# Performance work log

Hardware: AMD Instinct MI355X
Metric: run time of the kernel (lower is better)

The kernel has to match this reference:

```python
import jax, jax.numpy as jnp
import numpy as np

N = 8192       # number of nodes (dense NxN attention)
F_IN = 256     # input feature dim
F_OUT = 64     # projected feature dim (F_prime)
NEG_SLOPE = 0.01  # nn.LeakyReLU default


def setup_inputs() -> dict:
    key = jax.random.key(0)
    k0, k1, k2, k3 = jax.random.split(key, 4)
    H = jax.random.normal(k0, (N, F_IN), dtype=jnp.float32)
    # dense 0/1 adjacency; force self-loops so every row has a nonzero denominator
    A = jax.random.randint(k1, (N, N), 0, 2, dtype=jnp.int32)
    A = jnp.maximum(A, jnp.eye(N, dtype=jnp.int32))
    # learned params: W : F_IN -> F_OUT (self.W), a : 2*F_OUT -> 1 (self.a)
    W = jax.random.normal(k2, (F_IN, F_OUT), dtype=jnp.float32) / np.sqrt(F_IN)
    bW = jnp.zeros((F_OUT,), dtype=jnp.float32)
    a_w = jax.random.normal(k3, (2 * F_OUT,), dtype=jnp.float32) / np.sqrt(2 * F_OUT)
    a_b = jnp.zeros((), dtype=jnp.float32)
    return {"H": H, "A": A, "W": W, "bW": bW, "a_w": a_w, "a_b": a_b}


def reference(H, A, W, bW, a_w, a_b):
    # Wh[i] = W(H[i])  -> [N, F_OUT]
    Wh = H @ W + bW
    # a([Wh_i ; Wh_j]) = a1.Wh_i + a2.Wh_j + a_b : decompose the concat-linear
    s_src = Wh @ a_w[:F_OUT]           # [N]
    s_tar = Wh @ a_w[F_OUT:]           # [N]
    logits = s_src[:, None] + s_tar[None, :] + a_b   # [N, N]
    # e_ij = exp(leaky_relu(logits))
    e = jnp.exp(jnp.where(logits >= 0, logits, NEG_SLOPE * logits))
    # denominator masks by adjacency (sum_j e_ij * A_ij), as in the original
    denom = jnp.sum(e * A.astype(e.dtype), axis=1, keepdims=True)  # [N, 1]
    alpha = e / denom                   # NOTE: numerator NOT masked (faithful)
    # H'_i = sigmoid(alpha_i @ Wh)
    return jax.nn.sigmoid(alpha @ Wh)   # [N, F_OUT]
```

## Files before the change

### kernel.cpp

```cpp
#include <hip/hip_runtime.h>
#include <hip/hip_bf16.h>

#define NN 8192
#define FIN 256
#define FOUT 64

__global__ __launch_bounds__(256) void k1_proj(
    const float* __restrict__ H, const float* __restrict__ W,
    const float* __restrict__ bW, const float* __restrict__ aw,
    const float* __restrict__ ab,
    float* __restrict__ Wh, float* __restrict__ s_src, float* __restrict__ t_tar,
    float* __restrict__ E1, float* __restrict__ E2, float* __restrict__ PP)
{
    __shared__ float Hs[16 * FIN];
    int tid = threadIdx.x;
    int i0 = blockIdx.x * 16;
    const float4* Hv = (const float4*)(H + (size_t)i0 * FIN);
    float4* Hsv = (float4*)Hs;
    for (int idx = tid; idx < 16 * FIN / 4; idx += 256) Hsv[idx] = Hv[idx];
    __syncthreads();
    int f = tid & 63, sub = tid >> 6;
    float a1f = aw[f], a2f = aw[64 + f];
    float b = bW[f];
    float acc0 = b, acc1 = b, acc2 = b, acc3 = b;
    for (int k = 0; k < FIN; ++k) {
        float w = W[k * FOUT + f];
        acc0 += Hs[(sub     ) * FIN + k] * w;
        acc1 += Hs[(sub +  4) * FIN + k] * w;
        acc2 += Hs[(sub +  8) * FIN + k] * w;
        acc3 += Hs[(sub + 12) * FIN + k] * w;
    }
    float accs[4] = {acc0, acc1, acc2, acc3};
    #pragma unroll
    for (int q = 0; q < 4; ++q) {
        int i = i0 + sub + 4 * q;
        float a = accs[q];
        Wh[(size_t)i * FOUT + f] = a;
        float v1 = a * a1f, v2 = a * a2f;
        #pragma unroll
        for (int o = 32; o > 0; o >>= 1) {
            v1 += __shfl_xor(v1, o);
            v2 += __shfl_xor(v2, o);
        }
        if (f == 0) {
            float s = v1 + ab[0];
            float t = v2;
            s_src[i] = s; t_tar[i] = t;
            E1[i] = __expf(s); E2[i] = __expf(0.01f * s);
            PP[2 * i]     = __expf(t);
            PP[2 * i + 1] = __expf(0.01f * t);
        }
    }
}

__global__ __launch_bounds__(256) void k2_rank(
    const float* __restrict__ t_tar, const float* __restrict__ s_src,
    int* __restrict__ sorted_idx, int* __restrict__ kidx)
{
    __shared__ float Ts[NN];
    int tid = threadIdx.x;
    const float4* tv = (const float4*)t_tar;
    float4* Tsv = (float4*)Ts;
    for (int idx = tid; idx < NN / 4; idx += 256) Tsv[idx] = tv[idx];
    __syncthreads();
    int wv = tid >> 6, lane = tid & 63;
    int g = blockIdx.x * 4 + wv;
    float tj = Ts[g];
    float thr = -s_src[g];
    int rank = 0, kc = 0;
    #pragma unroll 4
    for (int k = lane; k < NN; k += 64) {
        float tk = Ts[k];
        rank += (tk < tj || (tk == tj && k < g)) ? 1 : 0;
        kc   += (tk < thr) ? 1 : 0;
    }
    #pragma unroll
    for (int o = 32; o > 0; o >>= 1) {
        rank += __shfl_xor(rank, o);
        kc   += __shfl_xor(kc, o);
    }
    if (lane == 0) { sorted_idx[rank] = g; kidx[g] = kc; }
}

__global__ __launch_bounds__(64) void k3a_tots(
    const float* __restrict__ Wh, const float* __restrict__ PP,
    const int* __restrict__ sorted_idx,
    float* __restrict__ tots1, float* __restrict__ tots2)
{
    int c = blockIdx.x, f = threadIdx.x;
    float t1 = 0.f, t2 = 0.f;
    int m0 = c * 32;
    #pragma unroll 8
    for (int m = m0; m < m0 + 32; ++m) {
        int sj = sorted_idx[m];
        float wh = Wh[(size_t)sj * 64 + f];
        t1 += PP[2 * sj]     * wh;
        t2 += PP[2 * sj + 1] * wh;
    }
    tots1[c * 64 + f] = t1; tots2[c * 64 + f] = t2;
}

__global__ __launch_bounds__(1024) void k3b_scan(
    const float* __restrict__ tots1, const float* __restrict__ tots2,
    float* __restrict__ off1, float* __restrict__ off2,
    float* __restrict__ pre2, float* __restrict__ suf1)
{
    __shared__ float w1[16 * 64], w2[16 * 64];
    int tid = threadIdx.x, f = tid & 63, wv = tid >> 6;
    int c0 = wv * 16;
    float s1 = 0.f, s2 = 0.f;
    for (int c = c0; c < c0 + 16; ++c) { s1 += tots1[c * 64 + f]; s2 += tots2[c * 64 + f]; }
    w1[wv * 64 + f] = s1; w2[wv * 64 + f] = s2;
    __syncthreads();
    float o2 = 0.f;
    #pragma unroll
    for (int w = 0; w < 16; ++w) if (w < wv) o2 += w2[w * 64 + f];
    float run2 = o2;
    for (int c = c0; c < c0 + 16; ++c) { off2[c * 64 + f] = run2; run2 += tots2[c * 64 + f]; }
    if (wv == 15) pre2[(size_t)NN * 64 + f] = run2;
    float o1 = 0.f;
    #pragma unroll
    for (int w = 0; w < 16; ++w) if (w > wv) o1 += w1[w * 64 + f];
    float run1 = o1;
    for (int c = c0 + 15; c >= c0; --c) { off1[c * 64 + f] = run1; run1 += tots1[c * 64 + f]; }
    if (tid < 64) suf1[(size_t)NN * 64 + tid] = 0.f;
}

__global__ __launch_bounds__(64) void k3c_emit(
    const float* __restrict__ Wh, const float* __restrict__ PP,
    const int* __restrict__ sorted_idx,
    const float* __restrict__ off1, const float* __restrict__ off2,
    float* __restrict__ pre2, float* __restrict__ suf1)
{
    int c = blockIdx.x, f = threadIdx.x;
    int m0 = c * 32;
    float whr[32], p1r[32], p2r[32];
    #pragma unroll
    for (int q = 0; q < 32; ++q) {
        int sj = sorted_idx[m0 + q];
        whr[q] = Wh[(size_t)sj * 64 + f];
        p1r[q] = PP[2 * sj]; p2r[q] = PP[2 * sj + 1];
    }
    float run2 = off2[c * 64 + f];
    #pragma unroll
    for (int q = 0; q < 32; ++q) {
        pre2[(size_t)(m0 + q) * 64 + f] = run2;
        run2 += p2r[q] * whr[q];
    }
    float run1 = off1[c * 64 + f];
    #pragma unroll
    for (int q = 31; q >= 0; --q) {
        run1 += p1r[q] * whr[q];
        suf1[(size_t)(m0 + q) * 64 + f] = run1;
    }
}

__global__ __launch_bounds__(256) void k4_denom(
    const int* __restrict__ A, const float* __restrict__ PP,
    const float* __restrict__ E1, const float* __restrict__ E2,
    float* __restrict__ denom)
{
    int tid = threadIdx.x;
    int i0 = blockIdx.x * 8;
    float e1r[8], accA[8], accB[8];
    #pragma unroll
    for (int r = 0; r < 8; ++r) { e1r[r] = E1[i0 + r]; accA[r] = 0.f; accB[r] = 0.f; }
    const float4* PPv = (const float4*)PP;
    for (int jv = tid; jv < NN / 4; jv += 256) {
        float4 ppA = PPv[2 * jv];
        float4 ppB = PPv[2 * jv + 1];
        #pragma unroll
        for (int r = 0; r < 8; ++r) {
            const int4 a4 = *(const int4*)(A + (size_t)(i0 + r) * NN + jv * 4);
            float e1 = e1r[r];
            {
                bool c = e1 * ppA.x >= 1.0f;
                float af = (float)a4.x;
                accA[r] += af * (c ? ppA.x : 0.0f);
                accB[r] += af * (c ? 0.0f : ppA.y);
            }
            {
                bool c = e1 * ppA.z >= 1.0f;
                float af = (float)a4.y;
                accA[r] += af * (c ? ppA.z : 0.0f);
                accB[r] += af * (c ? 0.0f : ppA.w);
            }
            {
                bool c = e1 * ppB.x >= 1.0f;
                float af = (float)a4.z;
                accA[r] += af * (c ? ppB.x : 0.0f);
                accB[r] += af * (c ? 0.0f : ppB.y);
            }
            {
                bool c = e1 * ppB.z >= 1.0f;
                float af = (float)a4.w;
                accA[r] += af * (c ? ppB.z : 0.0f);
                accB[r] += af * (c ? 0.0f : ppB.w);
            }
        }
    }
    #pragma unroll
    for (int r = 0; r < 8; ++r) {
        #pragma unroll
        for (int o = 32; o > 0; o >>= 1) {
            accA[r] += __shfl_xor(accA[r], o);
            accB[r] += __shfl_xor(accB[r], o);
        }
    }
    __shared__ float red[4][8][2];
    int wv = tid >> 6;
    if ((tid & 63) == 0) {
        #pragma unroll
        for (int r = 0; r < 8; ++r) { red[wv][r][0] = accA[r]; red[wv][r][1] = accB[r]; }
    }
    __syncthreads();
    if (tid < 8) {
        float sA = red[0][tid][0] + red[1][tid][0] + red[2][tid][0] + red[3][tid][0];
        float sB = red[0][tid][1] + red[1][tid][1] + red[2][tid][1] + red[3][tid][1];
        denom[i0 + tid] = E1[i0 + tid] * sA + E2[i0 + tid] * sB;
    }
}

__global__ __launch_bounds__(256) void k5_out(
    const float* __restrict__ suf1, const float* __restrict__ pre2,
    const int* __restrict__ kidx, const float* __restrict__ E1,
    const float* __restrict__ E2, const float* __restrict__ denom,
    float* __restrict__ out)
{
    int tid = threadIdx.x;
    int f = tid & 63, sub = tid >> 6;
    int i = blockIdx.x * 4 + sub;
    int k = kidx[i];
    float num = E1[i] * suf1[(size_t)k * 64 + f] + E2[i] * pre2[(size_t)k * 64 + f];
    float x = num / denom[i];
    out[(size_t)i * 64 + f] = 1.0f / (1.0f + __expf(-x));
}

extern "C" void kernel_launch(void* const* d_in, const int* in_sizes, int n_in,
                              void* d_out, int out_size, void* d_ws, size_t ws_size,
                              hipStream_t stream) {
    const float* H  = (const float*)d_in[0];
    const int*   A  = (const int*)d_in[1];
    const float* W  = (const float*)d_in[2];
    const float* bW = (const float*)d_in[3];
    const float* aw = (const float*)d_in[4];
    const float* ab = (const float*)d_in[5];
    float* out = (float*)d_out;

    float* ws    = (float*)d_ws;
    float* Wh    = ws;
    float* s_src = Wh + 524288;
    float* t_tar = s_src + 8192;
    float* E1    = t_tar + 8192;
    float* E2    = E1 + 8192;
    float* PP    = E2 + 8192;
    float* denom = PP + 16384;
    float* pre2  = denom + 8192;
    float* suf1  = pre2 + 524352;
    float* tots1 = suf1 + 524352;
    float* tots2 = tots1 + 16384;
    float* off1  = tots2 + 16384;
    float* off2  = off1 + 16384;
    int* sorted_idx = (int*)(off2 + 16384);
    int* kidx       = sorted_idx + 8192;

    hipLaunchKernelGGL(k1_proj, dim3(512), dim3(256), 0, stream,
                       H, W, bW, aw, ab, Wh, s_src, t_tar, E1, E2, PP);
    hipLaunchKernelGGL(k2_rank, dim3(2048), dim3(256), 0, stream,
                       t_tar, s_src, sorted_idx, kidx);
    hipLaunchKernelGGL(k3a_tots, dim3(256), dim3(64), 0, stream,
                       Wh, PP, sorted_idx, tots1, tots2);
    hipLaunchKernelGGL(k3b_scan, dim3(1), dim3(1024), 0, stream,
                       tots1, tots2, off1, off2, pre2, suf1);
    hipLaunchKernelGGL(k3c_emit, dim3(256), dim3(64), 0, stream,
                       Wh, PP, sorted_idx, off1, off2, pre2, suf1);
    hipLaunchKernelGGL(k4_denom, dim3(1024), dim3(256), 0, stream,
                       A, PP, E1, E2, denom);
    hipLaunchKernelGGL(k5_out, dim3(2048), dim3(256), 0, stream,
                       suf1, pre2, kidx, E1, E2, denom, out);
}
```

Baseline: 415.6 us.

## Fuse scan into emit and denom into output, use nontemporal adjacency loads

The single-block scan kernel is removed: each emit block now computes its own prefix and suffix offsets by summing the chunk totals directly. The denominator and output kernels are merged, with the denominator passed through shared memory. The rank kernel handles two targets per wave, halving its grid. Adjacency loads become nontemporal. Together these cut kernel launches and serialisation, at the cost of redundant O(256) offset sums in each emit block. The dominant cost, the 256 MB adjacency read, is unchanged.

New measurement: 409.7 us. About the same (-1.4%).

```diff
diff --git a/kernel.cpp b/kernel.cpp
--- a/kernel.cpp
+++ b/kernel.cpp
@@ -4,6 +4,8 @@
 #define NN 8192
 #define FIN 256
 #define FOUT 64
+
+typedef int iv4 __attribute__((ext_vector_type(4)));
 
 __global__ __launch_bounds__(256) void k1_proj(
     const float* __restrict__ H, const float* __restrict__ W,
@@ -64,22 +66,28 @@
     for (int idx = tid; idx < NN / 4; idx += 256) Tsv[idx] = tv[idx];
     __syncthreads();
     int wv = tid >> 6, lane = tid & 63;
-    int g = blockIdx.x * 4 + wv;
-    float tj = Ts[g];
-    float thr = -s_src[g];
-    int rank = 0, kc = 0;
+    int gA = blockIdx.x * 8 + wv * 2;
+    int gB = gA + 1;
+    float tjA = Ts[gA], tjB = Ts[gB];
+    float thrA = -s_src[gA], thrB = -s_src[gB];
+    int rA = 0, kA = 0, rB = 0, kB = 0;
     #pragma unroll 4
     for (int k = lane; k < NN; k += 64) {
         float tk = Ts[k];
-        rank += (tk < tj || (tk == tj && k < g)) ? 1 : 0;
-        kc   += (tk < thr) ? 1 : 0;
+        rA += (tk < tjA || (tk == tjA && k < gA)) ? 1 : 0;
+        kA += (tk < thrA) ? 1 : 0;
+        rB += (tk < tjB || (tk == tjB && k < gB)) ? 1 : 0;
+        kB += (tk < thrB) ? 1 : 0;
     }
     #pragma unroll
     for (int o = 32; o > 0; o >>= 1) {
-        rank += __shfl_xor(rank, o);
-        kc   += __shfl_xor(kc, o);
-    }
-    if (lane == 0) { sorted_idx[rank] = g; kidx[g] = kc; }
+        rA += __shfl_xor(rA, o); kA += __shfl_xor(kA, o);
+        rB += __shfl_xor(rB, o); kB += __shfl_xor(kB, o);
+    }
+    if (lane == 0) {
+        sorted_idx[rA] = gA; kidx[gA] = kA;
+        sorted_idx[rB] = gB; kidx[gB] = kB;
+    }
 }
 
 __global__ __launch_bounds__(64) void k3a_tots(
@@ -100,39 +108,19 @@
     tots1[c * 64 + f] = t1; tots2[c * 64 + f] = t2;
 }
 
-__global__ __launch_bounds__(1024) void k3b_scan(
-    const float* __restrict__ tots1, const float* __restrict__ tots2,
-    float* __restrict__ off1, float* __restrict__ off2,
-    float* __restrict__ pre2, float* __restrict__ suf1)
-{
-    __shared__ float w1[16 * 64], w2[16 * 64];
-    int tid = threadIdx.x, f = tid & 63, wv = tid >> 6;
-    int c0 = wv * 16;
-    float s1 = 0.f, s2 = 0.f;
-    for (int c = c0; c < c0 + 16; ++c) { s1 += tots1[c * 64 + f]; s2 += tots2[c * 64 + f]; }
-    w1[wv * 64 + f] = s1; w2[wv * 64 + f] = s2;
-    __syncthreads();
-    float o2 = 0.f;
-    #pragma unroll
-    for (int w = 0; w < 16; ++w) if (w < wv) o2 += w2[w * 64 + f];
-    float run2 = o2;
-    for (int c = c0; c < c0 + 16; ++c) { off2[c * 64 + f] = run2; run2 += tots2[c * 64 + f]; }
-    if (wv == 15) pre2[(size_t)NN * 64 + f] = run2;
-    float o1 = 0.f;
-    #pragma unroll
-    for (int w = 0; w < 16; ++w) if (w > wv) o1 += w1[w * 64 + f];
-    float run1 = o1;
-    for (int c = c0 + 15; c >= c0; --c) { off1[c * 64 + f] = run1; run1 += tots1[c * 64 + f]; }
-    if (tid < 64) suf1[(size_t)NN * 64 + tid] = 0.f;
-}
-
-__global__ __launch_bounds__(64) void k3c_emit(
+__global__ __launch_bounds__(64) void k3bc_emit(
     const float* __restrict__ Wh, const float* __restrict__ PP,
     const int* __restrict__ sorted_idx,
-    const float* __restrict__ off1, const float* __restrict__ off2,
+    const float* __restrict__ tots1, const float* __restrict__ tots2,
     float* __restrict__ pre2, float* __restrict__ suf1)
 {
     int c = blockIdx.x, f = threadIdx.x;
+    float o2 = 0.f;
+    #pragma unroll 8
+    for (int w = 0; w < c; ++w) o2 += tots2[w * 64 + f];
+    float o1 = 0.f;
+    #pragma unroll 8
+    for (int w = c + 1; w < 256; ++w) o1 += tots1[w * 64 + f];
     int m0 = c * 32;
     float whr[32], p1r[32], p2r[32];
     #pragma unroll
@@ -141,24 +129,27 @@
         whr[q] = Wh[(size_t)sj * 64 + f];
         p1r[q] = PP[2 * sj]; p2r[q] = PP[2 * sj + 1];
     }
-    float run2 = off2[c * 64 + f];
+    float run2 = o2;
     #pragma unroll
     for (int q = 0; q < 32; ++q) {
         pre2[(size_t)(m0 + q) * 64 + f] = run2;
         run2 += p2r[q] * whr[q];
     }
-    float run1 = off1[c * 64 + f];
+    if (c == 255) pre2[(size_t)NN * 64 + f] = run2;
+    float run1 = o1;
     #pragma unroll
     for (int q = 31; q >= 0; --q) {
         run1 += p1r[q] * whr[q];
         suf1[(size_t)(m0 + q) * 64 + f] = run1;
     }
-}
-
-__global__ __launch_bounds__(256) void k4_denom(
+    if (c == 255) suf1[(size_t)NN * 64 + f] = 0.f;
+}
+
+__global__ __launch_bounds__(256) void k45_denom_out(
     const int* __restrict__ A, const float* __restrict__ PP,
     const float* __restrict__ E1, const float* __restrict__ E2,
-    float* __restrict__ denom)
+    const float* __restrict__ suf1, const float* __restrict__ pre2,
+    const int* __restrict__ kidx, float* __restrict__ out)
 {
     int tid = threadIdx.x;
     int i0 = blockIdx.x * 8;
@@ -171,7 +162,8 @@
         float4 ppB = PPv[2 * jv + 1];
         #pragma unroll
         for (int r = 0; r < 8; ++r) {
-            const int4 a4 = *(const int4*)(A + (size_t)(i0 + r) * NN + jv * 4);
+            const iv4 a4 = __builtin_nontemporal_load(
+                (const iv4*)(A + (size_t)(i0 + r) * NN + jv * 4));
             float e1 = e1r[r];
             {
                 bool c = e1 * ppA.x >= 1.0f;
@@ -208,6 +200,7 @@
         }
     }
     __shared__ float red[4][8][2];
+    __shared__ float sden[8];
     int wv = tid >> 6;
     if ((tid & 63) == 0) {
         #pragma unroll
@@ -217,23 +210,19 @@
     if (tid < 8) {
         float sA = red[0][tid][0] + red[1][tid][0] + red[2][tid][0] + red[3][tid][0];
         float sB = red[0][tid][1] + red[1][tid][1] + red[2][tid][1] + red[3][tid][1];
-        denom[i0 + tid] = E1[i0 + tid] * sA + E2[i0 + tid] * sB;
-    }
-}
-
-__global__ __launch_bounds__(256) void k5_out(
-    const float* __restrict__ suf1, const float* __restrict__ pre2,
-    const int* __restrict__ kidx, const float* __restrict__ E1,
-    const float* __restrict__ E2, const float* __restrict__ denom,
-    float* __restrict__ out)
-{
-    int tid = threadIdx.x;
+        sden[tid] = E1[i0 + tid] * sA + E2[i0 + tid] * sB;
+    }
+    __syncthreads();
     int f = tid & 63, sub = tid >> 6;
-    int i = blockIdx.x * 4 + sub;
-    int k = kidx[i];
-    float num = E1[i] * suf1[(size_t)k * 64 + f] + E2[i] * pre2[(size_t)k * 64 + f];
-    float x = num / denom[i];
-    out[(size_t)i * 64 + f] = 1.0f / (1.0f + __expf(-x));
+    #pragma unroll
+    for (int rr = 0; rr < 2; ++rr) {
+        int r = sub + 4 * rr;
+        int i = i0 + r;
+        int k = kidx[i];
+        float num = E1[i] * suf1[(size_t)k * 64 + f] + E2[i] * pre2[(size_t)k * 64 + f];
+        float x = num / sden[r];
+        out[(size_t)i * 64 + f] = 1.0f / (1.0f + __expf(-x));
+    }
 }
 
 extern "C" void kernel_launch(void* const* d_in, const int* in_sizes, int n_in,
@@ -254,28 +243,21 @@
     float* E1    = t_tar + 8192;
     float* E2    = E1 + 8192;
     float* PP    = E2 + 8192;
-    float* denom = PP + 16384;
-    float* pre2  = denom + 8192;
+    float* pre2  = PP + 16384;
     float* suf1  = pre2 + 524352;
     float* tots1 = suf1 + 524352;
     float* tots2 = tots1 + 16384;
-    float* off1  = tots2 + 16384;
-    float* off2  = off1 + 16384;
-    int* sorted_idx = (int*)(off2 + 16384);
+    int* sorted_idx = (int*)(tots2 + 16384);
     int* kidx       = sorted_idx + 8192;
 
     hipLaunchKernelGGL(k1_proj, dim3(512), dim3(256), 0, stream,
                        H, W, bW, aw, ab, Wh, s_src, t_tar, E1, E2, PP);
-    hipLaunchKernelGGL(k2_rank, dim3(2048), dim3(256), 0, stream,
+    hipLaunchKernelGGL(k2_rank, dim3(1024), dim3(256), 0, stream,
                        t_tar, s_src, sorted_idx, kidx);
     hipLaunchKernelGGL(k3a_tots, dim3(256), dim3(64), 0, stream,
                        Wh, PP, sorted_idx, tots1, tots2);
-    hipLaunchKernelGGL(k3b_scan, dim3(1), dim3(1024), 0, stream,
-                       tots1, tots2, off1, off2, pre2, suf1);
-    hipLaunchKernelGGL(k3c_emit, dim3(256), dim3(64), 0, stream,
-                       Wh, PP, sorted_idx, off1, off2, pre2, suf1);
-    hipLaunchKernelGGL(k4_denom, dim3(1024), dim3(256), 0, stream,
-                       A, PP, E1, E2, denom);
-    hipLaunchKernelGGL(k5_out, dim3(2048), dim3(256), 0, stream,
-                       suf1, pre2, kidx, E1, E2, denom, out);
-}
+    hipLaunchKernelGGL(k3bc_emit, dim3(256), dim3(64), 0, stream,
+                       Wh, PP, sorted_idx, tots1, tots2, pre2, suf1);
+    hipLaunchKernelGGL(k45_denom_out, dim3(1024), dim3(256), 0, stream,
+                       A, PP, E1, E2, suf1, pre2, kidx, out);
+}
```
